# Kernel optimization log

Hardware: AMD Instinct MI355X
Metric: run time of the kernel (lower is better)

The kernel has to match this reference:

```python
import jax, jax.numpy as jnp
import numpy as np

EPS = 1e-12  # matches torch.nn.functional.normalize eps

def _l2norm(x, axis=-1):
    n = jnp.sqrt(jnp.sum(x * x, axis=axis, keepdims=True))
    return x / jnp.maximum(n, EPS)

def setup_inputs() -> dict:
    key = jax.random.key(0)
    k1, k2 = jax.random.split(key)
    B, C, H, W = 16, 256, 32, 32
    K = 8192
    z = jax.random.normal(k1, (B, C, H, W), dtype=jnp.float32)
    # torch init: uniform(-1/K, 1/K)
    emb_weight = jax.random.uniform(k2, (K, C), dtype=jnp.float32,
                                    minval=-1.0 / K, maxval=1.0 / K)
    return {"z": z, "emb_weight": emb_weight}

def reference(z, emb_weight):
    B, C, H, W = z.shape
    zt = jnp.transpose(z, (0, 2, 3, 1))            # [B,H,W,C]
    z_flat = zt.reshape(-1, C)                      # [N,C]
    zf_n = _l2norm(z_flat)                          # normalized tokens
    e_n = _l2norm(emb_weight)                       # normalized codebook [K,C]
    # squared euclidean distance via matmul (N x K)
    d = (jnp.sum(zf_n * zf_n, axis=1, keepdims=True)
         + jnp.sum(e_n * e_n, axis=1)
         - 2.0 * jnp.einsum('nc,kc->nk', zf_n, e_n))
    idx = jnp.argmin(d, axis=1)                     # [N]
    # get_codebook_entry: gather raw weight then normalize
    zq = _l2norm(emb_weight[idx])                   # [N,C]
    zq = zq.reshape(B, H, W, C)
    z_n = _l2norm(zt)                               # normalize z over channel dim
    # straight-through estimator
    zq = z_n + jax.lax.stop_gradient(zq - z_n)
    out = jnp.transpose(zq, (0, 3, 1, 2))           # [B,C,H,W]
    indices = idx.reshape(B, H, W)
    return out, indices
```

## Files before the change

kernel.cpp:

```cpp
#include <hip/hip_runtime.h>
#include <math.h>
#include <float.h>

#define K_CODES 8192
#define C_DIM   256
#define N_TOK   16384
#define B_      16
#define H_      32
#define W_      32
#define HW      1024
#define KSPLIT  16
#define TOKS_PER_BLK 128

typedef short  short8   __attribute__((ext_vector_type(8)));
typedef float  floatx16 __attribute__((ext_vector_type(16)));

__device__ inline ushort f32_to_bf16_rne(float x) {
    union { float f; unsigned u; } v; v.f = x;
    unsigned u = v.u;
    return (ushort)((u + 0x7FFFu + ((u >> 16) & 1u)) >> 16);
}
__device__ inline float bf16_bits_to_f32(ushort h) {
    union { unsigned u; float f; } v; v.u = ((unsigned)h) << 16;
    return v.f;
}
__device__ inline unsigned umax_(unsigned a, unsigned b) { return a > b ? a : b; }
__device__ inline unsigned umin_(unsigned a, unsigned b) { return a < b ? a : b; }

__device__ inline void g2l16(const void* g, void* l) {
    __builtin_amdgcn_global_load_lds((const __attribute__((address_space(1))) unsigned int*)g,
                                     (__attribute__((address_space(3))) unsigned int*)l,
                                     16, 0, 0);
}


__global__ __launch_bounds__(256) void norm_pack(
        const float* __restrict__ emb, const float* __restrict__ z,
        float* __restrict__ e_n, float* __restrict__ s2,
        ushort* __restrict__ Chi,
        float* __restrict__ ztn, ushort* __restrict__ Thi) {
    __shared__ float tile[32][257];
    __shared__ float pvt[32][9];
    __shared__ float pvt2[32][9];
    __shared__ float inv[32];
    int t = threadIdx.x;
    int bid = blockIdx.x;
    if (bid < 256) {
        int k0 = bid * 32;
        int r = t >> 3, cp = t & 7;
        const float* src = emb + (size_t)(k0 + r) * C_DIM + cp * 32;
        float ss = 0.f;
        #pragma unroll
        for (int j = 0; j < 8; ++j) {
            float4 v = *(const float4*)(src + j * 4);
            tile[r][cp * 32 + j * 4 + 0] = v.x;
            tile[r][cp * 32 + j * 4 + 1] = v.y;
            tile[r][cp * 32 + j * 4 + 2] = v.z;
            tile[r][cp * 32 + j * 4 + 3] = v.w;
            ss = fmaf(v.x, v.x, ss); ss = fmaf(v.y, v.y, ss);
            ss = fmaf(v.z, v.z, ss); ss = fmaf(v.w, v.w, ss);
        }
        pvt[r][cp] = ss;
        __syncthreads();
        if (t < 32) {
            float a = 0.f;
            #pragma unroll
            for (int p = 0; p < 8; ++p) a += pvt[t][p];
            inv[t] = 1.0f / fmaxf(sqrtf(a), 1e-12f);
        }
        __syncthreads();
        float iv = inv[r];
        float s2p = 0.f;
        float* dst = e_n + (size_t)(k0 + r) * C_DIM + cp * 32;
        #pragma unroll
        for (int j = 0; j < 8; ++j) {
            float a = tile[r][cp * 32 + j * 4 + 0] * iv;
            float b = tile[r][cp * 32 + j * 4 + 1] * iv;
            float c = tile[r][cp * 32 + j * 4 + 2] * iv;
            float d = tile[r][cp * 32 + j * 4 + 3] * iv;
            s2p = fmaf(a, a, s2p); s2p = fmaf(b, b, s2p);
            s2p = fmaf(c, c, s2p); s2p = fmaf(d, d, s2p);
            float4 o = {a, b, c, d};
            *(float4*)(dst + j * 4) = o;
        }
        pvt2[r][cp] = s2p;
        __syncthreads();
        if (t < 32) {
            float a = 0.f;
            #pragma unroll
            for (int p = 0; p < 8; ++p) a += pvt2[t][p];
            s2[k0 + t] = a;
        }
        char* chiB = (char*)Chi;
        #pragma unroll
        for (int e = 0; e < 4; ++e) {
            int p = e * 256 + t;
            int row = p & 31;
            int ch0 = ((p >> 6) << 4) | (((p >> 5) & 1) << 3);
            float rv = inv[row];
            union { ushort u[8]; uint4 v; } hs;
            #pragma unroll
            for (int i = 0; i < 8; ++i)
                hs.u[i] = f32_to_bf16_rne(tile[row][ch0 + i] * rv);
            size_t addr = (size_t)bid * 16384 + (size_t)p * 16;
            *(uint4*)(chiB + addr) = hs.v;
        }
    } else {
        int tb = bid - 256;
        int b = tb >> 5, h = tb & 31;
        const float* zb = z + ((size_t)(b * C_DIM) * H_ + h) * W_;
        int c0 = t >> 3, wq = t & 7;
        #pragma unroll
        for (int it = 0; it < 8; ++it) {
            int c = it * 32 + c0;
            float4 v = *(const float4*)(zb + (size_t)c * HW + wq * 4);
            tile[wq * 4 + 0][c] = v.x;
            tile[wq * 4 + 1][c] = v.y;
            tile[wq * 4 + 2][c] = v.z;
            tile[wq * 4 + 3][c] = v.w;
        }
        __syncthreads();
        int part = t >> 5, w2 = t & 31;
        float s = 0.f;
        #pragma unroll
        for (int i = 0; i < 32; ++i) {
            float v = tile[w2][part * 32 + i];
            s = fmaf(v, v, s);
        }
        pvt[w2][part] = s;
        __syncthreads();
        if (t < 32) {
            float ss = 0.f;
            #pragma unroll
            for (int p = 0; p < 8; ++p) ss += pvt[t][p];
            inv[t] = 1.0f / fmaxf(sqrtf(ss), 1e-12f);
        }
        __syncthreads();
        int n_base = tb * 32;
        for (int r = 0; r < 32; ++r) {
            float val = tile[r][t] * inv[r];
            ztn[(size_t)(n_base + r) * C_DIM + t] = val;
        }
        char* thiB = (char*)Thi;
        #pragma unroll
        for (int e = 0; e < 4; ++e) {
            int p = e * 256 + t;
            int row = p & 31;
            int ch0 = ((p >> 6) << 4) | (((p >> 5) & 1) << 3);
            float rv = inv[row];
            union { ushort u[8]; uint4 v; } hs;
            #pragma unroll
            for (int i = 0; i < 8; ++i)
                hs.u[i] = f32_to_bf16_rne(tile[row][ch0 + i] * rv);
            size_t addr = (size_t)tb * 16384 + (size_t)p * 16;
            *(uint4*)(thiB + addr) = hs.v;
        }
    }
}

__global__ __launch_bounds__(256, 4) void score_topk(
        const ushort* __restrict__ Chi,
        const ushort* __restrict__ Thi, uint2* __restrict__ cand) {
    __shared__ __align__(16) char smem[16384];
    int t = threadIdx.x;
    int l = t & 63, wv = t >> 6;
    int hh = l >> 5, col = l & 31;
    int wr = wv >> 1, wc = wv & 1;
    int tokBase = blockIdx.x * TOKS_PER_BLK;
    int tokRG = tokBase >> 5;
    int part = blockIdx.y;
    int partBase = part * (K_CODES / KSPLIT);
    int codeRGbase = partBase >> 5;

    const char* chiB = (const char*)Chi;
    const char* thiB = (const char*)Thi;

    const char* gp[2];
    int ldo[2];
    int dkt[2];
    #pragma unroll
    for (int gi = 0; gi < 2; ++gi) {
        int sl = wv * 2 + gi;
        if (sl < 4) {
            gp[gi]  = chiB + (size_t)(codeRGbase + sl) * 16384 + (l << 4);
            ldo[gi] = sl << 10;
            dkt[gi] = 4 * 16384 - 15 * 1024;
        } else {
            int trg = sl - 4;
            gp[gi]  = thiB + (size_t)(tokRG + trg) * 16384 + (l << 4);
            ldo[gi] = 4096 + (trg << 10);
            dkt[gi] = -15 * 1024;
        }
    }
    auto issue = [&](int parity) {
        char* base = smem + (parity ? 8192 : 0);
        g2l16(gp[0], base + ldo[0]);
        g2l16(gp[1], base + ldo[1]);
    };
    auto advance = [&](int snum) {
        bool kb = (snum & 15) == 15;
        gp[0] += kb ? dkt[0] : 1024;
        gp[1] += kb ? dkt[1] : 1024;
    };

    issue(0); advance(0);

    unsigned rv1[2] = {0u, 0u}, rv2[2] = {0u, 0u}, rv3[2] = {0u, 0u};
    int ri1[2] = {0, 0}, ri2[2] = {0, 0}, ri3[2] = {0, 0};

    for (int kt = 0; kt < 4; ++kt) {
        floatx16 acc[2][2];
        #pragma unroll
        for (int ct = 0; ct < 2; ++ct)
            #pragma unroll
            for (int nt = 0; nt < 2; ++nt)
                #pragma unroll
                for (int r = 0; r < 16; ++r) acc[ct][nt][r] = 0.f;

        for (int ss = 0; ss < 16; ++ss) {
            int g = kt * 16 + ss;
            __syncthreads();
            if (g + 1 < 64) { issue((g + 1) & 1); advance(g + 1); }
            const char* buf = smem + ((g & 1) ? 8192 : 0);

            short8 ah0 = *(const short8*)(buf + (((wc << 1) | 0) << 10) + (l << 4));
            short8 ah1 = *(const short8*)(buf + (((wc << 1) | 1) << 10) + (l << 4));
            short8 bh0 = *(const short8*)(buf + 4096 + (((wr << 1) | 0) << 10) + (l << 4));
            short8 bh1 = *(const short8*)(buf + 4096 + (((wr << 1) | 1) << 10) + (l << 4));
            acc[0][0] = __builtin_amdgcn_mfma_f32_32x32x16_bf16(ah0, bh0, acc[0][0], 0, 0, 0);
            acc[0][1] = __builtin_amdgcn_mfma_f32_32x32x16_bf16(ah0, bh1, acc[0][1], 0, 0, 0);
            acc[1][0] = __builtin_amdgcn_mfma_f32_32x32x16_bf16(ah1, bh0, acc[1][0], 0, 0, 0);
            acc[1][1] = __builtin_amdgcn_mfma_f32_32x32x16_bf16(ah1, bh1, acc[1][1], 0, 0, 0);
        }

        int kbase = partBase + kt * 128;
        #pragma unroll
        for (int nt = 0; nt < 2; ++nt) {
            unsigned m1 = 0u, m2 = 0u, m3 = 0u;
            #pragma unroll
            for (int ct = 0; ct < 2; ++ct) {
                #pragma unroll
                for (int r = 0; r < 16; ++r) {
                    unsigned key = (__float_as_uint(fmaf(acc[ct][nt][r], 0.25f, 1.25f)) & 0xFFFFFFC0u)
                                   | (unsigned)(((((wc << 1) | ct)) << 4) | r);
                    unsigned t1 = umin_(m1, key); m1 = umax_(m1, key);
                    unsigned t2 = umin_(m2, t1);  m2 = umax_(m2, t1);
                    m3 = umax_(m3, t2);
                }
            }
            unsigned mm[3] = {m1, m2, m3};
            #pragma unroll
            for (int j = 0; j < 3; ++j) {
                unsigned k = mm[j];
                int o = (int)(k & 63u), r = o & 15;
                int c = kbase + ((o >> 4) << 5) + (r & 3) + 8 * (r >> 2) + 4 * hh;
                if (k > rv1[nt]) {
                    rv3[nt] = rv2[nt]; ri3[nt] = ri2[nt];
                    rv2[nt] = rv1[nt]; ri2[nt] = ri1[nt];
                    rv1[nt] = k; ri1[nt] = c;
                } else if (k > rv2[nt]) {
                    rv3[nt] = rv2[nt]; ri3[nt] = ri2[nt];
                    rv2[nt] = k; ri2[nt] = c;
                } else if (k > rv3[nt]) {
                    rv3[nt] = k; ri3[nt] = c;
                }
            }
        }
    }

    __syncthreads();
    unsigned* mk = (unsigned*)smem;
    int*      mi = (int*)(smem + 8192);
    #pragma unroll
    for (int nt = 0; nt < 2; ++nt) {
        int base = (wr * 64 + nt * 32 + col) * 12 + (((wc << 1) | hh)) * 3;
        mk[base + 0] = rv1[nt]; mi[base + 0] = ri1[nt];
        mk[base + 1] = rv2[nt]; mi[base + 1] = ri2[nt];
        mk[base + 2] = rv3[nt]; mi[base + 2] = ri3[nt];
    }
    __syncthreads();
    if (t < 128) {
        unsigned b1 = 0u, b2 = 0u, b3 = 0u;
        int i1 = 0x7FFFFFFF, i2 = 0x7FFFFFFF, i3 = 0x7FFFFFFF;
        #pragma unroll
        for (int j = 0; j < 12; ++j) {
            unsigned k = mk[t * 12 + j]; int i = mi[t * 12 + j];
            if (k > b1 || (k == b1 && i < i1)) {
                b3 = b2; i3 = i2; b2 = b1; i2 = i1; b1 = k; i1 = i;
            } else if (k > b2 || (k == b2 && i < i2)) {
                b3 = b2; i3 = i2; b2 = k; i2 = i;
            } else if (k > b3 || (k == b3 && i < i3)) {
                b3 = k; i3 = i;
            }
        }
        size_t base = ((size_t)part * N_TOK + tokBase + t) * 3;
        cand[base + 0] = {b1, (unsigned)i1};
        cand[base + 1] = {b2, (unsigned)i2};
        cand[base + 2] = {b3, (unsigned)i3};
    }
}

__global__ __launch_bounds__(256) void rescore_gather(
        const float* __restrict__ ztn, const float* __restrict__ e_n,
        const float* __restrict__ s2, const uint2* __restrict__ cand,
        float* __restrict__ out, float* __restrict__ idxf) {
    __shared__ __align__(16) char sm[32 * 257 * 4];
    __shared__ uint2 cd[32][48];
    __shared__ int idxs[32];
    __shared__ int slowlist[32];
    __shared__ unsigned bkey[32];
    __shared__ int nslow;
    float* tile = (float*)sm;
    int t = threadIdx.x;
    int bid = blockIdx.x;
    int b = bid >> 5, h = bid & 31;
    int n_base = bid * 32;
    int wv = t >> 6, l = t & 63;

    if (t == 0) nslow = 0;
    {
        int tok = t >> 3, p = t & 7;
        int n = n_base + tok;
        #pragma unroll
        for (int slot = 0; slot < 3; ++slot) {
            cd[tok][p * 3 + slot]        = cand[((size_t)p * N_TOK + n) * 3 + slot];
            cd[tok][(p + 8) * 3 + slot]  = cand[((size_t)(p + 8) * N_TOK + n) * 3 + slot];
        }
    }
    __syncthreads();

    if (t < 32) {
        unsigned b1k = 0u, b2k = 0u; int b1i = 0x7FFFFFFF, b2i = 0x7FFFFFFF;
        #pragma unroll
        for (int p = 0; p < 48; ++p) {
            uint2 c2 = cd[t][p];
            unsigned k = c2.x; int i = (int)c2.y;
            if (k > b1k || (k == b1k && i < b1i)) { b2k = b1k; b2i = b1i; b1k = k; b1i = i; }
            else if (k > b2k || (k == b2k && i < b2i)) { b2k = k; b2i = i; }
        }
        bkey[t] = b1k;
        if (b1k - b2k > 2048u) {
            idxs[t] = b1i;
            idxf[n_base + t] = (float)b1i;
        } else {
            int s = atomicAdd(&nslow, 1);
            slowlist[s] = t;
        }
    }
    __syncthreads();
    int ns = nslow;
    for (int j = wv; j < ns; j += 4) {
        int tok = slowlist[j];
        int n = n_base + tok;
        unsigned bk = bkey[tok];
        float bs = FLT_MAX; int bi = 0x7FFFFFFF;
        if (l < 48) {
            uint2 c2 = cd[tok][l];
            if (c2.x + 8192u >= bk) {
                int c = (int)c2.y;
                const float* er = e_n + (size_t)c * C_DIM;
                const float* zr = ztn + (size_t)n * C_DIM;
                float s = 0.f;
                #pragma unroll
                for (int jj = 0; jj < 64; ++jj) {
                    float4 e4 = *(const float4*)(er + jj * 4);
                    float4 z4 = *(const float4*)(zr + jj * 4);
                    s = fmaf(e4.x, z4.x, s); s = fmaf(e4.y, z4.y, s);
                    s = fmaf(e4.z, z4.z, s); s = fmaf(e4.w, z4.w, s);
                }
                bs = s2[c] - 2.f * s;
                bi = c;
            }
        }
        #pragma unroll
        for (int d = 1; d < 64; d <<= 1) {
            float os = __shfl_xor(bs, d);
            int   oi = __shfl_xor(bi, d);
            if (os < bs || (os == bs && oi < bi)) { bs = os; bi = oi; }
        }
        if (l == 0) { idxs[tok] = bi; idxf[n] = (float)bi; }
    }
    __syncthreads();

    for (int r = 0; r < 32; ++r) {
        int k = idxs[r];
        tile[r * 257 + t] = e_n[(size_t)k * C_DIM + t];
    }
    __syncthreads();
    int w = t & 31, c0 = t >> 5;
    float* ob = out + ((size_t)(b * C_DIM) * H_ + h) * W_;
    #pragma unroll
    for (int it = 0; it < 32; ++it) {
        int c = it * 8 + c0;
        ob[(size_t)c * HW + w] = tile[w * 257 + c];
    }
}

extern "C" void kernel_launch(void* const* d_in, const int* in_sizes, int n_in,
                              void* d_out, int out_size, void* d_ws, size_t ws_size,
                              hipStream_t stream) {
    const float* z   = (const float*)d_in[0];
    const float* emb = (const float*)d_in[1];
    float* out  = (float*)d_out;
    float* idxf = out + (size_t)B_ * C_DIM * H_ * W_;

    char* ws = (char*)d_ws;
    size_t o = 0;
    float*  e_n  = (float*)(ws + o);  o += (size_t)K_CODES * C_DIM * 4;
    float*  s2   = (float*)(ws + o);  o += 32768;
    float*  ztn  = (float*)(ws + o);  o += (size_t)N_TOK * C_DIM * 4;
    ushort* Chi  = (ushort*)(ws + o); o += (size_t)K_CODES * C_DIM * 2;
    ushort* Thi  = (ushort*)(ws + o); o += (size_t)N_TOK * C_DIM * 2;
    uint2*  cand = (uint2*)(ws + o);  o += (size_t)KSPLIT * N_TOK * 3 * 8;

    hipLaunchKernelGGL(norm_pack, dim3(256 + B_ * H_), dim3(256), 0, stream,
                       emb, z, e_n, s2, Chi, ztn, Thi);
    hipLaunchKernelGGL(score_topk, dim3(N_TOK / TOKS_PER_BLK, KSPLIT), dim3(256), 0, stream,
                       Chi, Thi, cand);
    hipLaunchKernelGGL(rescore_gather, dim3(B_ * H_), dim3(256), 0, stream,
                       ztn, e_n, s2, cand, out, idxf);
}
```

Before: 208.4 us.

## Enlarge score_topk tiles and use a 5-slot async LDS pipeline

The score kernel now uses 512-thread blocks, each covering 256 tokens by 256 codes per pass, with 8 waves each computing a 2x4 grid of 32x32 MFMA tiles. Staging becomes a 5-slot ring of 16KB LDS buffers that stays three loads ahead, using explicit vmcnt waits and raw barriers in place of double buffering with __syncthreads, plus s_setprio around the MFMA bursts. The aim is better data reuse per LDS load and hiding global-to-LDS latency. In exchange it uses 80KB of LDS per block, which limits occupancy, and more accumulator registers per wave.

```diff
diff --git a/kernel.cpp b/kernel.cpp
--- a/kernel.cpp
+++ b/kernel.cpp
@@ -10,7 +10,6 @@
 #define W_      32
 #define HW      1024
 #define KSPLIT  16
-#define TOKS_PER_BLK 128
 
 typedef short  short8   __attribute__((ext_vector_type(8)));
 typedef float  floatx16 __attribute__((ext_vector_type(16)));
@@ -19,10 +18,6 @@
     union { float f; unsigned u; } v; v.f = x;
     unsigned u = v.u;
     return (ushort)((u + 0x7FFFu + ((u >> 16) & 1u)) >> 16);
-}
-__device__ inline float bf16_bits_to_f32(ushort h) {
-    union { unsigned u; float f; } v; v.u = ((unsigned)h) << 16;
-    return v.f;
 }
 __device__ inline unsigned umax_(unsigned a, unsigned b) { return a > b ? a : b; }
 __device__ inline unsigned umin_(unsigned a, unsigned b) { return a < b ? a : b; }
@@ -158,15 +153,15 @@
     }
 }
 
-__global__ __launch_bounds__(256, 4) void score_topk(
+__global__ __launch_bounds__(512, 2) void score_topk(
         const ushort* __restrict__ Chi,
         const ushort* __restrict__ Thi, uint2* __restrict__ cand) {
-    __shared__ __align__(16) char smem[16384];
+    __shared__ __align__(16) char smem[81920];
     int t = threadIdx.x;
     int l = t & 63, wv = t >> 6;
     int hh = l >> 5, col = l & 31;
-    int wr = wv >> 1, wc = wv & 1;
-    int tokBase = blockIdx.x * TOKS_PER_BLK;
+    int wr = wv >> 2, wc = wv & 3;
+    int tokBase = blockIdx.x * 256;
     int tokRG = tokBase >> 5;
     int part = blockIdx.y;
     int partBase = part * (K_CODES / KSPLIT);
@@ -176,115 +171,132 @@
     const char* thiB = (const char*)Thi;
 
     const char* gp[2];
-    int ldo[2];
     int dkt[2];
     #pragma unroll
     for (int gi = 0; gi < 2; ++gi) {
         int sl = wv * 2 + gi;
-        if (sl < 4) {
+        if (sl < 8) {
             gp[gi]  = chiB + (size_t)(codeRGbase + sl) * 16384 + (l << 4);
-            ldo[gi] = sl << 10;
-            dkt[gi] = 4 * 16384 - 15 * 1024;
+            dkt[gi] = 8 * 16384 - 15 * 1024;
         } else {
-            int trg = sl - 4;
-            gp[gi]  = thiB + (size_t)(tokRG + trg) * 16384 + (l << 4);
-            ldo[gi] = 4096 + (trg << 10);
+            gp[gi]  = thiB + (size_t)(tokRG + (sl - 8)) * 16384 + (l << 4);
             dkt[gi] = -15 * 1024;
         }
     }
-    auto issue = [&](int parity) {
-        char* base = smem + (parity ? 8192 : 0);
-        g2l16(gp[0], base + ldo[0]);
-        g2l16(gp[1], base + ldo[1]);
-    };
-    auto advance = [&](int snum) {
-        bool kb = (snum & 15) == 15;
+    int ldo0 = (wv * 2 + 0) << 10, ldo1 = (wv * 2 + 1) << 10;
+    int issueSlot = 0, ssIss = 0;
+    auto issueStage = [&]() {
+        char* base = smem + issueSlot * 16384;
+        g2l16(gp[0], base + ldo0);
+        g2l16(gp[1], base + ldo1);
+        bool kb = (ssIss & 15) == 15;
         gp[0] += kb ? dkt[0] : 1024;
         gp[1] += kb ? dkt[1] : 1024;
+        ++ssIss;
+        issueSlot = (issueSlot == 4) ? 0 : issueSlot + 1;
     };
 
-    issue(0); advance(0);
-
-    unsigned rv1[2] = {0u, 0u}, rv2[2] = {0u, 0u}, rv3[2] = {0u, 0u};
-    int ri1[2] = {0, 0}, ri2[2] = {0, 0}, ri3[2] = {0, 0};
-
-    for (int kt = 0; kt < 4; ++kt) {
-        floatx16 acc[2][2];
-        #pragma unroll
-        for (int ct = 0; ct < 2; ++ct)
-            #pragma unroll
-            for (int nt = 0; nt < 2; ++nt)
+    issueStage(); issueStage(); issueStage();
+    asm volatile("s_waitcnt vmcnt(4)" ::: "memory");
+    __builtin_amdgcn_s_barrier();
+
+    floatx16 acc[2][4];
+    #pragma unroll
+    for (int n = 0; n < 2; ++n)
+        #pragma unroll
+        for (int m = 0; m < 4; ++m)
+            #pragma unroll
+            for (int r = 0; r < 16; ++r) acc[n][m][r] = 0.f;
+
+    unsigned rv1[4] = {0u,0u,0u,0u}, rv2[4] = {0u,0u,0u,0u}, rv3[4] = {0u,0u,0u,0u};
+    int ri1[4] = {0,0,0,0}, ri2[4] = {0,0,0,0}, ri3[4] = {0,0,0,0};
+
+    int readSlot = 0;
+    for (int p = 0; p < 32; ++p) {
+        const char* buf = smem + readSlot * 16384;
+        short8 cf0 = *(const short8*)(buf + ((wc * 2 + 0) << 10) + (l << 4));
+        short8 cf1 = *(const short8*)(buf + ((wc * 2 + 1) << 10) + (l << 4));
+        short8 tf0 = *(const short8*)(buf + 8192 + ((wr * 4 + 0) << 10) + (l << 4));
+        short8 tf1 = *(const short8*)(buf + 8192 + ((wr * 4 + 1) << 10) + (l << 4));
+        short8 tf2 = *(const short8*)(buf + 8192 + ((wr * 4 + 2) << 10) + (l << 4));
+        short8 tf3 = *(const short8*)(buf + 8192 + ((wr * 4 + 3) << 10) + (l << 4));
+        if (p < 29) issueStage();
+        if (p < 29)      asm volatile("s_waitcnt vmcnt(4)" ::: "memory");
+        else if (p == 29) asm volatile("s_waitcnt vmcnt(2)" ::: "memory");
+        else if (p == 30) asm volatile("s_waitcnt vmcnt(0)" ::: "memory");
+        __builtin_amdgcn_s_barrier();
+        __builtin_amdgcn_s_setprio(1);
+        acc[0][0] = __builtin_amdgcn_mfma_f32_32x32x16_bf16(cf0, tf0, acc[0][0], 0, 0, 0);
+        acc[0][1] = __builtin_amdgcn_mfma_f32_32x32x16_bf16(cf0, tf1, acc[0][1], 0, 0, 0);
+        acc[0][2] = __builtin_amdgcn_mfma_f32_32x32x16_bf16(cf0, tf2, acc[0][2], 0, 0, 0);
+        acc[0][3] = __builtin_amdgcn_mfma_f32_32x32x16_bf16(cf0, tf3, acc[0][3], 0, 0, 0);
+        acc[1][0] = __builtin_amdgcn_mfma_f32_32x32x16_bf16(cf1, tf0, acc[1][0], 0, 0, 0);
+        acc[1][1] = __builtin_amdgcn_mfma_f32_32x32x16_bf16(cf1, tf1, acc[1][1], 0, 0, 0);
+        acc[1][2] = __builtin_amdgcn_mfma_f32_32x32x16_bf16(cf1, tf2, acc[1][2], 0, 0, 0);
+        acc[1][3] = __builtin_amdgcn_mfma_f32_32x32x16_bf16(cf1, tf3, acc[1][3], 0, 0, 0);
+        __builtin_amdgcn_s_setprio(0);
+        readSlot = (readSlot == 4) ? 0 : readSlot + 1;
+
+        if ((p & 15) == 15) {
+            int kb2 = partBase + (p >> 4) * 256 + wc * 64;
+            #pragma unroll
+            for (int m = 0; m < 4; ++m) {
+                unsigned m1 = 0u, m2 = 0u, m3 = 0u;
                 #pragma unroll
-                for (int r = 0; r < 16; ++r) acc[ct][nt][r] = 0.f;
-
-        for (int ss = 0; ss < 16; ++ss) {
-            int g = kt * 16 + ss;
-            __syncthreads();
-            if (g + 1 < 64) { issue((g + 1) & 1); advance(g + 1); }
-            const char* buf = smem + ((g & 1) ? 8192 : 0);
-
-            short8 ah0 = *(const short8*)(buf + (((wc << 1) | 0) << 10) + (l << 4));
-            short8 ah1 = *(const short8*)(buf + (((wc << 1) | 1) << 10) + (l << 4));
-            short8 bh0 = *(const short8*)(buf + 4096 + (((wr << 1) | 0) << 10) + (l << 4));
-            short8 bh1 = *(const short8*)(buf + 4096 + (((wr << 1) | 1) << 10) + (l << 4));
-            acc[0][0] = __builtin_amdgcn_mfma_f32_32x32x16_bf16(ah0, bh0, acc[0][0], 0, 0, 0);
-            acc[0][1] = __builtin_amdgcn_mfma_f32_32x32x16_bf16(ah0, bh1, acc[0][1], 0, 0, 0);
-            acc[1][0] = __builtin_amdgcn_mfma_f32_32x32x16_bf16(ah1, bh0, acc[1][0], 0, 0, 0);
-            acc[1][1] = __builtin_amdgcn_mfma_f32_32x32x16_bf16(ah1, bh1, acc[1][1], 0, 0, 0);
-        }
-
-        int kbase = partBase + kt * 128;
-        #pragma unroll
-        for (int nt = 0; nt < 2; ++nt) {
-            unsigned m1 = 0u, m2 = 0u, m3 = 0u;
-            #pragma unroll
-            for (int ct = 0; ct < 2; ++ct) {
+                for (int n = 0; n < 2; ++n) {
+                    #pragma unroll
+                    for (int r = 0; r < 16; ++r) {
+                        unsigned key = (__float_as_uint(fmaf(acc[n][m][r], 0.25f, 1.25f)) & 0xFFFFFFC0u)
+                                       | (unsigned)((n << 4) | r);
+                        unsigned t1 = umin_(m1, key); m1 = umax_(m1, key);
+                        unsigned t2 = umin_(m2, t1);  m2 = umax_(m2, t1);
+                        m3 = umax_(m3, t2);
+                    }
+                }
+                unsigned mm[3] = {m1, m2, m3};
                 #pragma unroll
-                for (int r = 0; r < 16; ++r) {
-                    unsigned key = (__float_as_uint(fmaf(acc[ct][nt][r], 0.25f, 1.25f)) & 0xFFFFFFC0u)
-                                   | (unsigned)(((((wc << 1) | ct)) << 4) | r);
-                    unsigned t1 = umin_(m1, key); m1 = umax_(m1, key);
-                    unsigned t2 = umin_(m2, t1);  m2 = umax_(m2, t1);
-                    m3 = umax_(m3, t2);
+                for (int j = 0; j < 3; ++j) {
+                    unsigned k = mm[j];
+                    int o = (int)(k & 63u), r = o & 15, n = o >> 4;
+                    int c = kb2 + (n << 5) + (r & 3) + 8 * (r >> 2) + 4 * hh;
+                    if (k > rv1[m]) {
+                        rv3[m] = rv2[m]; ri3[m] = ri2[m];
+                        rv2[m] = rv1[m]; ri2[m] = ri1[m];
+                        rv1[m] = k; ri1[m] = c;
+                    } else if (k > rv2[m]) {
+                        rv3[m] = rv2[m]; ri3[m] = ri2[m];
+                        rv2[m] = k; ri2[m] = c;
+                    } else if (k > rv3[m]) {
+                        rv3[m] = k; ri3[m] = c;
+                    }
                 }
             }
-            unsigned mm[3] = {m1, m2, m3};
-            #pragma unroll
-            for (int j = 0; j < 3; ++j) {
-                unsigned k = mm[j];
-                int o = (int)(k & 63u), r = o & 15;
-                int c = kbase + ((o >> 4) << 5) + (r & 3) + 8 * (r >> 2) + 4 * hh;
-                if (k > rv1[nt]) {
-                    rv3[nt] = rv2[nt]; ri3[nt] = ri2[nt];
-                    rv2[nt] = rv1[nt]; ri2[nt] = ri1[nt];
-                    rv1[nt] = k; ri1[nt] = c;
-                } else if (k > rv2[nt]) {
-                    rv3[nt] = rv2[nt]; ri3[nt] = ri2[nt];
-                    rv2[nt] = k; ri2[nt] = c;
-                } else if (k > rv3[nt]) {
-                    rv3[nt] = k; ri3[nt] = c;
-                }
-            }
+            #pragma unroll
+            for (int n = 0; n < 2; ++n)
+                #pragma unroll
+                for (int m = 0; m < 4; ++m)
+                    #pragma unroll
+                    for (int r = 0; r < 16; ++r) acc[n][m][r] = 0.f;
         }
     }
 
     __syncthreads();
     unsigned* mk = (unsigned*)smem;
-    int*      mi = (int*)(smem + 8192);
+    int*      mi = (int*)(smem + 24576);
     #pragma unroll
-    for (int nt = 0; nt < 2; ++nt) {
-        int base = (wr * 64 + nt * 32 + col) * 12 + (((wc << 1) | hh)) * 3;
-        mk[base + 0] = rv1[nt]; mi[base + 0] = ri1[nt];
-        mk[base + 1] = rv2[nt]; mi[base + 1] = ri2[nt];
-        mk[base + 2] = rv3[nt]; mi[base + 2] = ri3[nt];
-    }
-    __syncthreads();
-    if (t < 128) {
+    for (int m = 0; m < 4; ++m) {
+        int base = (wr * 128 + m * 32 + col) * 24 + ((wc << 1) | hh) * 3;
+        mk[base + 0] = rv1[m]; mi[base + 0] = ri1[m];
+        mk[base + 1] = rv2[m]; mi[base + 1] = ri2[m];
+        mk[base + 2] = rv3[m]; mi[base + 2] = ri3[m];
+    }
+    __syncthreads();
+    if (t < 256) {
         unsigned b1 = 0u, b2 = 0u, b3 = 0u;
         int i1 = 0x7FFFFFFF, i2 = 0x7FFFFFFF, i3 = 0x7FFFFFFF;
         #pragma unroll
-        for (int j = 0; j < 12; ++j) {
-            unsigned k = mk[t * 12 + j]; int i = mi[t * 12 + j];
+        for (int j = 0; j < 24; ++j) {
+            unsigned k = mk[t * 24 + j]; int i = mi[t * 24 + j];
             if (k > b1 || (k == b1 && i < i1)) {
                 b3 = b2; i3 = i2; b2 = b1; i2 = i1; b1 = k; i1 = i;
             } else if (k > b2 || (k == b2 && i < i2)) {
@@ -415,7 +427,7 @@
 
     hipLaunchKernelGGL(norm_pack, dim3(256 + B_ * H_), dim3(256), 0, stream,
                        emb, z, e_n, s2, Chi, ztn, Thi);
-    hipLaunchKernelGGL(score_topk, dim3(N_TOK / TOKS_PER_BLK, KSPLIT), dim3(256), 0, stream,
+    hipLaunchKernelGGL(score_topk, dim3(N_TOK / 256, KSPLIT), dim3(512), 0, stream,
                        Chi, Thi, cand);
     hipLaunchKernelGGL(rescore_gather, dim3(B_ * H_), dim3(256), 0, stream,
                        ztn, e_n, s2, cand, out, idxf);
```

New measurement: 214.1 us. 1.03x slower.
